# Kernel optimization log

Measured on AMD Instinct MI355X. Metric: run time of the kernel, lower is better.

## Reference

```python
import jax, jax.numpy as jnp
import numpy as np

B, S_REF, E, H = 128, 2048, 512, 512

def setup_inputs() -> dict:
    key = jax.random.key(0)
    ks = jax.random.split(key, 13)
    def lin(kw, kb, out_d, in_d):
        bound = 1.0 / np.sqrt(in_d)
        w = jax.random.uniform(kw, (out_d, in_d), minval=-bound, maxval=bound, dtype=jnp.float32)
        b = jax.random.uniform(kb, (out_d,), minval=-bound, maxval=bound, dtype=jnp.float32)
        return w, b
    Wa_w, Wa_b = lin(ks[0], ks[1], H, H)
    Ua_w, Ua_b = lin(ks[2], ks[3], H, H)
    Va_w, Va_b = lin(ks[4], ks[5], 1, H)
    Wih_w, Wih_b = lin(ks[6], ks[7], H, E + H)
    Whh_w, Whh_b = lin(ks[8], ks[9], H, H)
    x_t = jax.random.normal(ks[10], (B, 1, E), dtype=jnp.float32)
    x_ref_encoded = jax.random.normal(ks[11], (B, S_REF, H), dtype=jnp.float32)
    h_prev = jax.random.normal(ks[12], (B, H), dtype=jnp.float32)
    return {"x_t": x_t, "x_ref_encoded": x_ref_encoded, "h_prev": h_prev,
            "Wa_w": Wa_w, "Wa_b": Wa_b, "Ua_w": Ua_w, "Ua_b": Ua_b,
            "Va_w": Va_w, "Va_b": Va_b, "Wih_w": Wih_w, "Wih_b": Wih_b,
            "Whh_w": Whh_w, "Whh_b": Whh_b}

def reference(x_t, x_ref_encoded, h_prev, Wa_w, Wa_b, Ua_w, Ua_b, Va_w, Va_b, Wih_w, Wih_b, Whh_w, Whh_b):
    # Bahdanau additive attention
    q = h_prev @ Wa_w.T + Wa_b                      # (B, H)
    k = jnp.einsum('bsh,oh->bso', x_ref_encoded, Ua_w) + Ua_b  # (B, S, H)
    scores = jnp.einsum('bsh,h->bs', jnp.tanh(q[:, None, :] + k), Va_w[0]) + Va_b[0]  # (B, S)
    attn_weights = jax.nn.softmax(scores, axis=1)
    context = jnp.einsum('bs,bsh->bh', attn_weights, x_ref_encoded)  # (B, H)
    # Reservoir RNN cell on concat(x_t[:,0,:], context)
    rnn_in = jnp.concatenate([x_t[:, 0, :], context], axis=1)        # (B, E+H)
    h_next = jnp.tanh(rnn_in @ Wih_w.T + Wih_b + h_prev @ Whh_w.T + Whh_b)
    return (h_next, context)
```

## Files before the change

kernel.cpp:

```cpp
#include <hip/hip_runtime.h>
#include <hip/hip_bf16.h>
#include <math.h>


typedef __attribute__((ext_vector_type(8))) short short8;
typedef __attribute__((ext_vector_type(8))) unsigned short ushort8;
typedef __attribute__((ext_vector_type(4))) float f32x4;

#define S_LEN 2048
#define BDIM 128
#define HDIM 512
#define EDIM 512
#define BM 64
#define NCHUNK (S_LEN / BM)

__device__ __forceinline__ unsigned short f2bf(float f) {
  unsigned int u = __float_as_uint(f);
  u += 0x7fffu + ((u >> 16) & 1u);
  return (unsigned short)(u >> 16);
}

__device__ __forceinline__ float bf2f(unsigned short u) {
  return __uint_as_float(((unsigned int)u) << 16);
}

__device__ __forceinline__ float fast_tanh(float x) {
  float e = __expf(2.0f * x);
  return 1.0f - 2.0f / (e + 1.0f);
}

__global__ __launch_bounds__(256) void k_cvt_b(const float* __restrict__ src,
                                               unsigned short* __restrict__ dst) {
  int tid = blockIdx.x * 256 + threadIdx.x;
  int ct = tid >> 10;
  int kt = (tid >> 6) & 15;
  int l = tid & 63;
  int col = ct * 16 + (l & 15);
  int k = kt * 32 + (l >> 4) * 8;
  const float4* s = (const float4*)(src + (size_t)col * HDIM + k);
  float4 v0 = s[0], v1 = s[1];
  ushort8 p;
  p[0] = f2bf(v0.x); p[1] = f2bf(v0.y); p[2] = f2bf(v0.z); p[3] = f2bf(v0.w);
  p[4] = f2bf(v1.x); p[5] = f2bf(v1.y); p[6] = f2bf(v1.z); p[7] = f2bf(v1.w);
  *(ushort8*)(dst + (size_t)tid * 8) = p;
}

__global__ __launch_bounds__(256) void k_q(const float* __restrict__ hp,
                                           const float* __restrict__ Wa,
                                           const float* __restrict__ Wab,
                                           const float* __restrict__ Uab,
                                           float* __restrict__ q) {
  int b = blockIdx.x, oh = blockIdx.y;
  int o = oh * 256 + threadIdx.x;
  __shared__ float hs[HDIM];
  hs[threadIdx.x] = hp[b * HDIM + threadIdx.x];
  hs[threadIdx.x + 256] = hp[b * HDIM + threadIdx.x + 256];
  __syncthreads();
  const float4* wr = (const float4*)(Wa + (size_t)o * HDIM);
  float acc = 0.f;
#pragma unroll 8
  for (int i = 0; i < HDIM / 4; ++i) {
    float4 v = wr[i];
    acc += v.x * hs[i * 4 + 0] + v.y * hs[i * 4 + 1] + v.z * hs[i * 4 + 2] + v.w * hs[i * 4 + 3];
  }
  q[b * HDIM + o] = acc + Wab[o] + Uab[o];
}

__global__ __launch_bounds__(512, 4) void k_scores_ctx(
    const float* __restrict__ xref, const unsigned short* __restrict__ uab,
    const float* __restrict__ q, const float* __restrict__ va,
    float* __restrict__ mArr, float* __restrict__ lArr, float* __restrict__ cpart) {
  int chunk = blockIdx.x;
  int b = blockIdx.y;
  int tid = threadIdx.x;
  int l = tid & 63;
  int w = tid >> 6;
  int c = l & 15, g4 = l >> 4;

  __shared__ __align__(16) unsigned short As[BM * HDIM];
  __shared__ float sc[BM];
  __shared__ float pl[BM];

  f32x4 acc[4][4];
#pragma unroll
  for (int m = 0; m < 4; ++m)
#pragma unroll
    for (int n = 0; n < 4; ++n) acc[m][n] = f32x4{0.f, 0.f, 0.f, 0.f};

  const float* xb = xref + ((size_t)b * S_LEN + (size_t)chunk * BM) * HDIM;

  int srow = tid >> 3, skq = tid & 7;
  char* wb = (char*)&As[0] + srow * 1024 + ((skq * 16) ^ ((srow & 7) << 4));
  const float* sb = xb + (size_t)srow * HDIM + skq * 8;

  float4 a0, a1, a2, a3, a4, a5, a6, a7;

#define LD2(va, vb, p)                                                         \
  {                                                                            \
    va = *(const float4*)(sb + (p) * 64);                                      \
    vb = *(const float4*)(sb + (p) * 64 + 4);                                  \
  }

#define WR1(va, vb, p)                                                         \
  {                                                                            \
    union { __hip_bfloat162 h[4]; ushort8 s; } u_;                             \
    u_.h[0] = __float22bfloat162_rn(make_float2(va.x, va.y));                  \
    u_.h[1] = __float22bfloat162_rn(make_float2(va.z, va.w));                  \
    u_.h[2] = __float22bfloat162_rn(make_float2(vb.x, vb.y));                  \
    u_.h[3] = __float22bfloat162_rn(make_float2(vb.z, vb.w));                  \
    *(ushort8*)(wb + (p) * 128) = u_.s;                                        \
  }

#define CLUSTER(kt)                                                            \
  {                                                                            \
    short8 afr_[4], bfr_[4];                                                   \
    _Pragma("unroll")                                                          \
    for (int n = 0; n < 4; ++n) {                                              \
      int ct = w * 4 + n;                                                      \
      bfr_[n] = *(const short8*)(uab + (((size_t)(ct * 16 + (kt)) * 64 + l) * 8)); \
    }                                                                          \
    _Pragma("unroll")                                                          \
    for (int m = 0; m < 4; ++m) {                                              \
      int row = m * 16 + (l & 15);                                             \
      int kb = ((kt) * 64 + (l >> 4) * 16) ^ ((row & 7) << 4);                 \
      afr_[m] = *(const short8*)((const char*)&As[0] + row * 1024 + kb);       \
    }                                                                          \
    __builtin_amdgcn_s_setprio(1);                                             \
    _Pragma("unroll")                                                          \
    for (int m = 0; m < 4; ++m)                                                \
      _Pragma("unroll")                                                        \
      for (int n = 0; n < 4; ++n)                                              \
        acc[m][n] = __builtin_amdgcn_mfma_f32_16x16x32_bf16(afr_[m], bfr_[n],  \
                                                            acc[m][n], 0, 0, 0); \
    __builtin_amdgcn_s_setprio(0);                                             \
  }

  LD2(a0, a1, 0) LD2(a2, a3, 1) LD2(a4, a5, 2) LD2(a6, a7, 3)
  WR1(a0, a1, 0) WR1(a2, a3, 1) WR1(a4, a5, 2) WR1(a6, a7, 3)
  LD2(a0, a1, 4) LD2(a2, a3, 5) LD2(a4, a5, 6) LD2(a6, a7, 7)
  WR1(a0, a1, 4) WR1(a2, a3, 5) WR1(a4, a5, 6) WR1(a6, a7, 7)
  if (tid < BM) sc[tid] = 0.f;
  __syncthreads();

  CLUSTER(0)  CLUSTER(1)  CLUSTER(2)  CLUSTER(3)
  CLUSTER(4)  CLUSTER(5)  CLUSTER(6)  CLUSTER(7)
  CLUSTER(8)  CLUSTER(9)  CLUSTER(10) CLUSTER(11)
  CLUSTER(12) CLUSTER(13)

  float qf[4], vf[4];
#pragma unroll
  for (int n = 0; n < 4; ++n) {
    int o = w * 64 + n * 16 + c;
    qf[n] = q[b * HDIM + o];
    vf[n] = va[o];
  }
  CLUSTER(14) CLUSTER(15)

#pragma unroll
  for (int m = 0; m < 4; ++m) {
#pragma unroll
    for (int r = 0; r < 4; ++r) {
      float sum = 0.f;
#pragma unroll
      for (int n = 0; n < 4; ++n) sum += fast_tanh(acc[m][n][r] + qf[n]) * vf[n];
      sum += __shfl_xor(sum, 1);
      sum += __shfl_xor(sum, 2);
      sum += __shfl_xor(sum, 4);
      sum += __shfl_xor(sum, 8);
      if (c == 0) atomicAdd(&sc[m * 16 + g4 * 4 + r], sum);
    }
  }
  __syncthreads();

  float M = sc[l];
#pragma unroll
  for (int off = 32; off >= 1; off >>= 1) M = fmaxf(M, __shfl_xor(M, off));
  float pp = __expf(sc[l] - M);
  float lsum = pp;
#pragma unroll
  for (int off = 32; off >= 1; off >>= 1) lsum += __shfl_xor(lsum, off);
  if (tid < BM) pl[tid] = pp;
  if (tid == 0) {
    mArr[b * NCHUNK + chunk] = M;
    lArr[b * NCHUNK + chunk] = lsum;
  }
  __syncthreads();

  {
    int h2 = tid * 2;
    const char* base_ = (const char*)&As[0];
    float cacc = 0.f;
#pragma unroll 8
    for (int r = 0; r < BM; ++r) {
      int byte = r * 1024 + (h2 ^ ((r & 7) << 4));
      cacc += pl[r] * bf2f(*(const unsigned short*)(base_ + byte));
    }
    cpart[((size_t)b * NCHUNK + chunk) * HDIM + tid] = cacc;
  }
#undef LD2
#undef WR1
#undef CLUSTER
}

__global__ __launch_bounds__(512) void k_combine(const float* __restrict__ mArr,
                                                 const float* __restrict__ lArr,
                                                 const float* __restrict__ cpart,
                                                 float* __restrict__ ctx,
                                                 float* __restrict__ out_ctx) {
  int b = blockIdx.x, t = threadIdx.x;
  __shared__ float wf[NCHUNK];
  __shared__ float dinv;
  if (t == 0) {
    float M = mArr[b * NCHUNK];
    for (int i = 1; i < NCHUNK; ++i) M = fmaxf(M, mArr[b * NCHUNK + i]);
    float den = 0.f;
    for (int i = 0; i < NCHUNK; ++i) {
      float f = __expf(mArr[b * NCHUNK + i] - M);
      wf[i] = f;
      den += f * lArr[b * NCHUNK + i];
    }
    dinv = 1.0f / den;
  }
  __syncthreads();
  float s = 0.f;
#pragma unroll
  for (int i = 0; i < NCHUNK; ++i) s += wf[i] * cpart[((size_t)b * NCHUNK + i) * HDIM + t];
  float c = s * dinv;
  ctx[b * HDIM + t] = c;
  out_ctx[b * HDIM + t] = c;
}

__global__ __launch_bounds__(256) void k_rnn(const float* __restrict__ xt,
                                             const float* __restrict__ ctx,
                                             const float* __restrict__ hp,
                                             const float* __restrict__ Wih,
                                             const float* __restrict__ Wihb,
                                             const float* __restrict__ Whh,
                                             const float* __restrict__ Whhb,
                                             float* __restrict__ hout) {
  int b = blockIdx.x, oh = blockIdx.y;
  int o = oh * 256 + threadIdx.x;
  __shared__ float xs[EDIM], cs[HDIM], hs[HDIM];
  xs[threadIdx.x] = xt[b * EDIM + threadIdx.x];
  xs[threadIdx.x + 256] = xt[b * EDIM + threadIdx.x + 256];
  cs[threadIdx.x] = ctx[b * HDIM + threadIdx.x];
  cs[threadIdx.x + 256] = ctx[b * HDIM + threadIdx.x + 256];
  hs[threadIdx.x] = hp[b * HDIM + threadIdx.x];
  hs[threadIdx.x + 256] = hp[b * HDIM + threadIdx.x + 256];
  __syncthreads();
  const float4* wi = (const float4*)(Wih + (size_t)o * (EDIM + HDIM));
  float acc = Wihb[o] + Whhb[o];
#pragma unroll 8
  for (int i = 0; i < EDIM / 4; ++i) {
    float4 v = wi[i];
    acc += v.x * xs[i * 4] + v.y * xs[i * 4 + 1] + v.z * xs[i * 4 + 2] + v.w * xs[i * 4 + 3];
  }
  const float4* wi2 = wi + EDIM / 4;
#pragma unroll 8
  for (int i = 0; i < HDIM / 4; ++i) {
    float4 v = wi2[i];
    acc += v.x * cs[i * 4] + v.y * cs[i * 4 + 1] + v.z * cs[i * 4 + 2] + v.w * cs[i * 4 + 3];
  }
  const float4* wh = (const float4*)(Whh + (size_t)o * HDIM);
#pragma unroll 8
  for (int i = 0; i < HDIM / 4; ++i) {
    float4 v = wh[i];
    acc += v.x * hs[i * 4] + v.y * hs[i * 4 + 1] + v.z * hs[i * 4 + 2] + v.w * hs[i * 4 + 3];
  }
  hout[b * HDIM + o] = tanhf(acc);
}

extern "C" void kernel_launch(void* const* d_in, const int* in_sizes, int n_in,
                              void* d_out, int out_size, void* d_ws, size_t ws_size,
                              hipStream_t stream) {
  const float* x_t    = (const float*)d_in[0];
  const float* x_ref  = (const float*)d_in[1];
  const float* h_prev = (const float*)d_in[2];
  const float* Wa_w   = (const float*)d_in[3];
  const float* Wa_b   = (const float*)d_in[4];
  const float* Ua_w   = (const float*)d_in[5];
  const float* Ua_b   = (const float*)d_in[6];
  const float* Va_w   = (const float*)d_in[7];
  const float* Wih_w  = (const float*)d_in[9];
  const float* Wih_b  = (const float*)d_in[10];
  const float* Whh_w  = (const float*)d_in[11];
  const float* Whh_b  = (const float*)d_in[12];

  char* ws = (char*)d_ws;
  unsigned short* ua_fr = (unsigned short*)ws;
  float* q     = (float*)(ws + 524288);
  float* mArr  = (float*)(ws + 786432);
  float* lArr  = (float*)(ws + 802816);
  float* cpart = (float*)(ws + 819200);
  float* ctx   = (float*)(ws + 9207808);

  float* h_out   = (float*)d_out;
  float* ctx_out = h_out + BDIM * HDIM;

  k_cvt_b<<<dim3(128), dim3(256), 0, stream>>>(Ua_w, ua_fr);
  k_q<<<dim3(BDIM, 2), dim3(256), 0, stream>>>(h_prev, Wa_w, Wa_b, Ua_b, q);
  k_scores_ctx<<<dim3(NCHUNK, BDIM), dim3(512), 0, stream>>>(x_ref, ua_fr, q, Va_w, mArr, lArr, cpart);
  k_combine<<<dim3(BDIM), dim3(512), 0, stream>>>(mArr, lArr, cpart, ctx, ctx_out);
  k_rnn<<<dim3(BDIM, 2), dim3(256), 0, stream>>>(x_t, ctx, h_prev, Wih_w, Wih_b, Whh_w, Whh_b, h_out);
}
```

Measured before the change: 294.9 us.

## Make scores kernel persistent with double-buffered LDS and prefetched B fragments

The scores/context kernel now launches 256 blocks, each looping over 16 chunks of one batch row instead of one block per chunk. The next chunk's x_ref tile is loaded from global memory and converted into a second LDS buffer while MFMAs run on the current one. Ua fragments are register double-buffered across k-steps. This aims to hide global load latency and cut per-block launch and prologue cost, but it uses 128KB of LDS, lowers occupancy to one block per CU, and leaves only 256 blocks to spread across the GPU.

```diff
diff --git a/kernel.cpp b/kernel.cpp
--- a/kernel.cpp
+++ b/kernel.cpp
@@ -66,20 +66,22 @@
   q[b * HDIM + o] = acc + Wab[o] + Uab[o];
 }
 
-__global__ __launch_bounds__(512, 4) void k_scores_ctx(
+__global__ __launch_bounds__(512, 2) void k_scores_ctx(
     const float* __restrict__ xref, const unsigned short* __restrict__ uab,
     const float* __restrict__ q, const float* __restrict__ va,
     float* __restrict__ mArr, float* __restrict__ lArr, float* __restrict__ cpart) {
-  int chunk = blockIdx.x;
-  int b = blockIdx.y;
+  int p = blockIdx.x;
+  int b = p >> 1;
+  int chunk0 = (p & 1) * 16;
   int tid = threadIdx.x;
   int l = tid & 63;
   int w = tid >> 6;
   int c = l & 15, g4 = l >> 4;
 
-  __shared__ __align__(16) unsigned short As[BM * HDIM];
+  __shared__ __align__(16) unsigned short As[2][BM * HDIM];
   __shared__ float sc[BM];
   __shared__ float pl[BM];
+  char* lds0 = (char*)&As[0][0];
 
   f32x4 acc[4][4];
 #pragma unroll
@@ -87,65 +89,56 @@
 #pragma unroll
     for (int n = 0; n < 4; ++n) acc[m][n] = f32x4{0.f, 0.f, 0.f, 0.f};
 
-  const float* xb = xref + ((size_t)b * S_LEN + (size_t)chunk * BM) * HDIM;
-
   int srow = tid >> 3, skq = tid & 7;
-  char* wb = (char*)&As[0] + srow * 1024 + ((skq * 16) ^ ((srow & 7) << 4));
-  const float* sb = xb + (size_t)srow * HDIM + skq * 8;
+  int wboff = srow * 1024 + ((skq * 16) ^ ((srow & 7) << 4));
+  const float* xbase = xref + ((size_t)b * S_LEN + (size_t)chunk0 * BM + srow) * HDIM + skq * 8;
 
   float4 a0, a1, a2, a3, a4, a5, a6, a7;
-
-#define LD2(va, vb, p)                                                         \
+  short8 bA[4], bB[4];
+
+#define LD2(va, vb, src, pp_)                                                  \
   {                                                                            \
-    va = *(const float4*)(sb + (p) * 64);                                      \
-    vb = *(const float4*)(sb + (p) * 64 + 4);                                  \
-  }
-
-#define WR1(va, vb, p)                                                         \
+    va = *(const float4*)((src) + (pp_) * 64);                                 \
+    vb = *(const float4*)((src) + (pp_) * 64 + 4);                             \
+  }
+
+#define WR1(va, vb, nbuf, pp_)                                                 \
   {                                                                            \
     union { __hip_bfloat162 h[4]; ushort8 s; } u_;                             \
     u_.h[0] = __float22bfloat162_rn(make_float2(va.x, va.y));                  \
     u_.h[1] = __float22bfloat162_rn(make_float2(va.z, va.w));                  \
     u_.h[2] = __float22bfloat162_rn(make_float2(vb.x, vb.y));                  \
     u_.h[3] = __float22bfloat162_rn(make_float2(vb.z, vb.w));                  \
-    *(ushort8*)(wb + (p) * 128) = u_.s;                                        \
-  }
-
-#define CLUSTER(kt)                                                            \
+    *(ushort8*)((nbuf) + wboff + (pp_) * 128) = u_.s;                          \
+  }
+
+#define LOADB(dst, kt)                                                         \
   {                                                                            \
-    short8 afr_[4], bfr_[4];                                                   \
     _Pragma("unroll")                                                          \
-    for (int n = 0; n < 4; ++n) {                                              \
-      int ct = w * 4 + n;                                                      \
-      bfr_[n] = *(const short8*)(uab + (((size_t)(ct * 16 + (kt)) * 64 + l) * 8)); \
-    }                                                                          \
+    for (int n = 0; n < 4; ++n)                                                \
+      dst[n] = *(const short8*)(uab +                                          \
+               (((size_t)((w * 4 + n) * 16 + (kt)) * 64 + l) * 8));            \
+  }
+
+#define CLUSTERP(buse, bpre, cbuf, kt, ktn)                                    \
+  {                                                                            \
+    LOADB(bpre, ktn)                                                           \
+    short8 afr_[4];                                                            \
     _Pragma("unroll")                                                          \
     for (int m = 0; m < 4; ++m) {                                              \
       int row = m * 16 + (l & 15);                                             \
       int kb = ((kt) * 64 + (l >> 4) * 16) ^ ((row & 7) << 4);                 \
-      afr_[m] = *(const short8*)((const char*)&As[0] + row * 1024 + kb);       \
+      afr_[m] = *(const short8*)((cbuf) + row * 1024 + kb);                    \
     }                                                                          \
     __builtin_amdgcn_s_setprio(1);                                             \
     _Pragma("unroll")                                                          \
     for (int m = 0; m < 4; ++m)                                                \
       _Pragma("unroll")                                                        \
       for (int n = 0; n < 4; ++n)                                              \
-        acc[m][n] = __builtin_amdgcn_mfma_f32_16x16x32_bf16(afr_[m], bfr_[n],  \
+        acc[m][n] = __builtin_amdgcn_mfma_f32_16x16x32_bf16(afr_[m], buse[n],  \
                                                             acc[m][n], 0, 0, 0); \
     __builtin_amdgcn_s_setprio(0);                                             \
   }
-
-  LD2(a0, a1, 0) LD2(a2, a3, 1) LD2(a4, a5, 2) LD2(a6, a7, 3)
-  WR1(a0, a1, 0) WR1(a2, a3, 1) WR1(a4, a5, 2) WR1(a6, a7, 3)
-  LD2(a0, a1, 4) LD2(a2, a3, 5) LD2(a4, a5, 6) LD2(a6, a7, 7)
-  WR1(a0, a1, 4) WR1(a2, a3, 5) WR1(a4, a5, 6) WR1(a6, a7, 7)
-  if (tid < BM) sc[tid] = 0.f;
-  __syncthreads();
-
-  CLUSTER(0)  CLUSTER(1)  CLUSTER(2)  CLUSTER(3)
-  CLUSTER(4)  CLUSTER(5)  CLUSTER(6)  CLUSTER(7)
-  CLUSTER(8)  CLUSTER(9)  CLUSTER(10) CLUSTER(11)
-  CLUSTER(12) CLUSTER(13)
 
   float qf[4], vf[4];
 #pragma unroll
@@ -154,52 +147,94 @@
     qf[n] = q[b * HDIM + o];
     vf[n] = va[o];
   }
-  CLUSTER(14) CLUSTER(15)
-
-#pragma unroll
-  for (int m = 0; m < 4; ++m) {
-#pragma unroll
-    for (int r = 0; r < 4; ++r) {
-      float sum = 0.f;
-#pragma unroll
-      for (int n = 0; n < 4; ++n) sum += fast_tanh(acc[m][n][r] + qf[n]) * vf[n];
-      sum += __shfl_xor(sum, 1);
-      sum += __shfl_xor(sum, 2);
-      sum += __shfl_xor(sum, 4);
-      sum += __shfl_xor(sum, 8);
-      if (c == 0) atomicAdd(&sc[m * 16 + g4 * 4 + r], sum);
-    }
-  }
+
+  LOADB(bA, 0)
+  LD2(a0, a1, xbase, 0) LD2(a2, a3, xbase, 1) LD2(a4, a5, xbase, 2) LD2(a6, a7, xbase, 3)
+  WR1(a0, a1, lds0, 0) WR1(a2, a3, lds0, 1) WR1(a4, a5, lds0, 2) WR1(a6, a7, lds0, 3)
+  LD2(a0, a1, xbase, 4) LD2(a2, a3, xbase, 5) LD2(a4, a5, xbase, 6) LD2(a6, a7, xbase, 7)
+  WR1(a0, a1, lds0, 4) WR1(a2, a3, lds0, 5) WR1(a4, a5, lds0, 6) WR1(a6, a7, lds0, 7)
+  if (tid < BM) sc[tid] = 0.f;
   __syncthreads();
 
-  float M = sc[l];
-#pragma unroll
-  for (int off = 32; off >= 1; off >>= 1) M = fmaxf(M, __shfl_xor(M, off));
-  float pp = __expf(sc[l] - M);
-  float lsum = pp;
-#pragma unroll
-  for (int off = 32; off >= 1; off >>= 1) lsum += __shfl_xor(lsum, off);
-  if (tid < BM) pl[tid] = pp;
-  if (tid == 0) {
-    mArr[b * NCHUNK + chunk] = M;
-    lArr[b * NCHUNK + chunk] = lsum;
-  }
-  __syncthreads();
-
-  {
-    int h2 = tid * 2;
-    const char* base_ = (const char*)&As[0];
-    float cacc = 0.f;
-#pragma unroll 8
-    for (int r = 0; r < BM; ++r) {
-      int byte = r * 1024 + (h2 ^ ((r & 7) << 4));
-      cacc += pl[r] * bf2f(*(const unsigned short*)(base_ + byte));
-    }
-    cpart[((size_t)b * NCHUNK + chunk) * HDIM + tid] = cacc;
+  int cur = 0;
+#pragma unroll 1
+  for (int i = 0; i < 16; ++i) {
+    char* cbuf = lds0 + cur * 65536;
+    char* nbuf = lds0 + (cur ^ 1) * 65536;
+    const float* xnext = xbase + (size_t)(i + 1) * BM * HDIM;
+    bool notlast = (i < 15);
+
+    if (notlast) { LD2(a0, a1, xnext, 0) LD2(a2, a3, xnext, 1) LD2(a4, a5, xnext, 2) LD2(a6, a7, xnext, 3) }
+
+    CLUSTERP(bA, bB, cbuf, 0, 1)  CLUSTERP(bB, bA, cbuf, 1, 2)
+    CLUSTERP(bA, bB, cbuf, 2, 3)  CLUSTERP(bB, bA, cbuf, 3, 4)
+    CLUSTERP(bA, bB, cbuf, 4, 5)  CLUSTERP(bB, bA, cbuf, 5, 6)
+    CLUSTERP(bA, bB, cbuf, 6, 7)  CLUSTERP(bB, bA, cbuf, 7, 8)
+
+    if (notlast) {
+      WR1(a0, a1, nbuf, 0) WR1(a2, a3, nbuf, 1) WR1(a4, a5, nbuf, 2) WR1(a6, a7, nbuf, 3)
+      LD2(a0, a1, xnext, 4) LD2(a2, a3, xnext, 5) LD2(a4, a5, xnext, 6) LD2(a6, a7, xnext, 7)
+    }
+
+    CLUSTERP(bA, bB, cbuf, 8, 9)   CLUSTERP(bB, bA, cbuf, 9, 10)
+    CLUSTERP(bA, bB, cbuf, 10, 11) CLUSTERP(bB, bA, cbuf, 11, 12)
+    CLUSTERP(bA, bB, cbuf, 12, 13) CLUSTERP(bB, bA, cbuf, 13, 14)
+    CLUSTERP(bA, bB, cbuf, 14, 15) CLUSTERP(bB, bA, cbuf, 15, 0)
+
+    if (notlast) { WR1(a0, a1, nbuf, 4) WR1(a2, a3, nbuf, 5) WR1(a4, a5, nbuf, 6) WR1(a6, a7, nbuf, 7) }
+
+#pragma unroll
+    for (int m = 0; m < 4; ++m) {
+#pragma unroll
+      for (int r = 0; r < 4; ++r) {
+        float sum = 0.f;
+#pragma unroll
+        for (int n = 0; n < 4; ++n) sum += fast_tanh(acc[m][n][r] + qf[n]) * vf[n];
+        sum += __shfl_xor(sum, 1);
+        sum += __shfl_xor(sum, 2);
+        sum += __shfl_xor(sum, 4);
+        sum += __shfl_xor(sum, 8);
+        if (c == 0) atomicAdd(&sc[m * 16 + g4 * 4 + r], sum);
+      }
+    }
+#pragma unroll
+    for (int m = 0; m < 4; ++m)
+#pragma unroll
+      for (int n = 0; n < 4; ++n) acc[m][n] = f32x4{0.f, 0.f, 0.f, 0.f};
+    __syncthreads();
+
+    float M = sc[l];
+#pragma unroll
+    for (int off = 32; off >= 1; off >>= 1) M = fmaxf(M, __shfl_xor(M, off));
+    float pp = __expf(sc[l] - M);
+    float lsum = pp;
+#pragma unroll
+    for (int off = 32; off >= 1; off >>= 1) lsum += __shfl_xor(lsum, off);
+    if (tid < BM) pl[tid] = pp;
+    if (tid == 0) {
+      mArr[b * NCHUNK + chunk0 + i] = M;
+      lArr[b * NCHUNK + chunk0 + i] = lsum;
+    }
+    __syncthreads();
+    if (tid < BM) sc[tid] = 0.f;
+
+    {
+      int h2 = tid * 2;
+      float cacc = 0.f;
+#pragma unroll 8
+      for (int r = 0; r < BM; ++r) {
+        int byte = r * 1024 + (h2 ^ ((r & 7) << 4));
+        cacc += pl[r] * bf2f(*(const unsigned short*)(cbuf + byte));
+      }
+      cpart[((size_t)b * NCHUNK + chunk0 + i) * HDIM + tid] = cacc;
+    }
+    __syncthreads();
+    cur ^= 1;
   }
 #undef LD2
 #undef WR1
-#undef CLUSTER
+#undef LOADB
+#undef CLUSTERP
 }
 
 __global__ __launch_bounds__(512) void k_combine(const float* __restrict__ mArr,
@@ -299,7 +334,7 @@
 
   k_cvt_b<<<dim3(128), dim3(256), 0, stream>>>(Ua_w, ua_fr);
   k_q<<<dim3(BDIM, 2), dim3(256), 0, stream>>>(h_prev, Wa_w, Wa_b, Ua_b, q);
-  k_scores_ctx<<<dim3(NCHUNK, BDIM), dim3(512), 0, stream>>>(x_ref, ua_fr, q, Va_w, mArr, lArr, cpart);
+  k_scores_ctx<<<dim3(256), dim3(512), 0, stream>>>(x_ref, ua_fr, q, Va_w, mArr, lArr, cpart);
   k_combine<<<dim3(BDIM), dim3(512), 0, stream>>>(mArr, lArr, cpart, ctx, ctx_out);
   k_rnn<<<dim3(BDIM, 2), dim3(256), 0, stream>>>(x_t, ctx, h_prev, Wih_w, Wih_b, Whh_w, Whh_b, h_out);
 }
```

Result: slower. 570.2 us (+93.4%).
